# Performance work log

Hardware: AMD Instinct MI355X
Metric: run time of the kernel (lower is better)

The kernel has to match this reference:

```python
import jax, jax.numpy as jnp
import numpy as np

ENC = 1024
DEC = 1024


def setup_inputs() -> dict:
    key = jax.random.key(0)
    k = jax.random.split(key, 8)
    s1 = 1.0 / np.sqrt(ENC)
    s2 = 1.0 / np.sqrt(DEC)
    return {
        "encoder_outputs": jax.random.normal(k[0], (32, 2048, ENC), jnp.float32),
        "decoder_output": jax.random.normal(k[1], (32, 1, DEC), jnp.float32),
        "w1": jax.random.uniform(k[2], (ENC, ENC), jnp.float32, -s1, s1),
        "b1": jax.random.uniform(k[3], (ENC,), jnp.float32, -s1, s1),
        "w2": jax.random.uniform(k[4], (DEC, ENC), jnp.float32, -s2, s2),
        "b2": jax.random.uniform(k[5], (ENC,), jnp.float32, -s2, s2),
        "v": jax.random.uniform(k[6], (ENC, 1), jnp.float32, -s1, s1),
        "bv": jax.random.uniform(k[7], (1,), jnp.float32, -s1, s1),
    }


def reference(encoder_outputs, decoder_output, w1, b1, w2, b2, v, bv):
    # [B,1,E] query projection, broadcast-added to [B,S,E] key projection
    w2_dec = jnp.einsum("bqd,de->bqe", decoder_output, w2) + b2
    w1_enc = jnp.einsum("bsd,de->bse", encoder_outputs, w1) + b1
    scores = jnp.einsum("bse,eo->bso", jnp.tanh(w1_enc + w2_dec), v) + bv  # [B,S,1]
    attn = jax.nn.softmax(scores[..., 0], axis=1)  # softmax over sequence dim
    context = jnp.einsum("bs,bse->be", attn, encoder_outputs)  # [B,E]
    return context
```

## Files before the change

kernel.cpp:

```cpp
#include <hip/hip_runtime.h>
#include <hip/hip_bf16.h>


typedef __attribute__((ext_vector_type(8))) short short8;
typedef __attribute__((ext_vector_type(4))) float f32x4;

#define M_TOTAL 65536
#define KDIM    1024

static __device__ inline unsigned int pk2h(float a, float b) {
    unsigned int ua = __builtin_bit_cast(unsigned int, a) + 0x8000u;
    unsigned int ub = __builtin_bit_cast(unsigned int, b) + 0x8000u;
    return __builtin_amdgcn_perm(ub, ua, 0x07060302u);
}

static __device__ inline uint4 pkvec(float4 f0, float4 f1) {
    uint4 pv;
    pv.x = pk2h(f0.x, f0.y);
    pv.y = pk2h(f0.z, f0.w);
    pv.z = pk2h(f1.x, f1.y);
    pv.w = pk2h(f1.z, f1.w);
    return pv;
}

__global__ __launch_bounds__(64) void pack_w1(const float* __restrict__ w1,
                                              unsigned short* __restrict__ w1p) {
    const int nt = blockIdx.x;
    const int kt = blockIdx.y;
    const int l  = threadIdx.x;
    const int n  = nt * 16 + (l & 15);
    const int kb = kt * 32 + (l >> 4) * 8;
    const float* s = w1 + (size_t)kb * 1024 + n;
    uint4 wv;
    wv.x = pk2h(s[0],    s[1024]);
    wv.y = pk2h(s[2048], s[3072]);
    wv.z = pk2h(s[4096], s[5120]);
    wv.w = pk2h(s[6144], s[7168]);
    *reinterpret_cast<uint4*>(w1p + (((size_t)(kt * 64 + nt)) << 9) + (l << 3)) = wv;
}

__global__ __launch_bounds__(256) void qq_kern(const float* __restrict__ dec,
                                               const float* __restrict__ w2,
                                               const float* __restrict__ b1,
                                               const float* __restrict__ b2,
                                               float* __restrict__ qq) {
    const int b = blockIdx.y;
    const int e = blockIdx.x * 256 + threadIdx.x;
    const int d0 = blockIdx.z * 256;
    const float* db = dec + b * 1024;
    float acc = (blockIdx.z == 0) ? (b1[e] + b2[e]) : 0.f;
#pragma unroll 8
    for (int d = d0; d < d0 + 256; d++)
        acc = fmaf(db[d], w2[d * 1024 + e], acc);
    atomicAdd(&qq[b * 1024 + e], acc);
}

__global__ __launch_bounds__(512, 2) void score_gemm(const float* __restrict__ enc,
                                                     const unsigned short* __restrict__ w1p,
                                                     const float* __restrict__ qq,
                                                     const float* __restrict__ vvec,
                                                     float* __restrict__ scores) {
    __shared__ __align__(16) unsigned short As[2][64 * 256];

    const int m0 = blockIdx.x << 6;
    const int b = m0 >> 11;
    const int tid = threadIdx.x;
    const int wid = tid >> 6;
    const int lane = tid & 63;
    const int quad = lane >> 4, lc = lane & 15;

    const int sr  = tid >> 3;
    const int sc8 = tid & 7;
    const float* srcrow = enc + (size_t)(m0 + sr) * 1024 + (sc8 << 3);
    const int dstoff = (sr << 8) + ((sc8 ^ (sr & 7)) << 3);

    f32x4 acc[4][8];
#pragma unroll
    for (int mi = 0; mi < 4; mi++)
#pragma unroll
        for (int ni = 0; ni < 8; ni++)
            acc[mi][ni] = (f32x4){0.f, 0.f, 0.f, 0.f};

    const unsigned short* bb = w1p + ((size_t)wid << 12) + (lane << 3);

    short8 bA[8], bB[8];
#pragma unroll
    for (int ni = 0; ni < 8; ni++)
        bA[ni] = *reinterpret_cast<const short8*>(bb + ni * 512);

    {
        float4 f0 = *reinterpret_cast<const float4*>(srcrow);
        float4 f1 = *reinterpret_cast<const float4*>(srcrow + 4);
        float4 f2 = *reinterpret_cast<const float4*>(srcrow + 64);
        float4 f3 = *reinterpret_cast<const float4*>(srcrow + 68);
        *reinterpret_cast<uint4*>(&As[0][dstoff])      = pkvec(f0, f1);
        *reinterpret_cast<uint4*>(&As[0][dstoff + 64]) = pkvec(f2, f3);
        f0 = *reinterpret_cast<const float4*>(srcrow + 128);
        f1 = *reinterpret_cast<const float4*>(srcrow + 132);
        f2 = *reinterpret_cast<const float4*>(srcrow + 192);
        f3 = *reinterpret_cast<const float4*>(srcrow + 196);
        *reinterpret_cast<uint4*>(&As[0][dstoff + 128]) = pkvec(f0, f1);
        *reinterpret_cast<uint4*>(&As[0][dstoff + 192]) = pkvec(f2, f3);
    }
    __syncthreads();

    for (int c = 0; c < 4; ++c) {
        const unsigned short* Ar = As[c & 1];
        unsigned short* Aw = const_cast<unsigned short*>(As[(c & 1) ^ 1]);
        const int more = (c < 3);
        const float* snext = srcrow + ((c + 1) << 8);

        float4 fv0, fv1, fv2, fv3;
        if (more) {
            fv0 = *reinterpret_cast<const float4*>(snext);
            fv1 = *reinterpret_cast<const float4*>(snext + 4);
            fv2 = *reinterpret_cast<const float4*>(snext + 64);
            fv3 = *reinterpret_cast<const float4*>(snext + 68);
        }

#pragma unroll
        for (int half = 0; half < 2; ++half) {
#pragma unroll
            for (int it = 0; it < 2; ++it) {
                const int lk = half * 4 + it * 2;
                const int kt = c * 8 + lk;
#pragma unroll
                for (int ni = 0; ni < 8; ni++)
                    bB[ni] = *reinterpret_cast<const short8*>(bb + (kt + 1) * 32768 + ni * 512);

                short8 af[4];
                {
                    const int cc = lk * 4 + quad;
                    const int off = ((cc & ~7) | ((cc ^ lc) & 7)) << 3;
#pragma unroll
                    for (int mi = 0; mi < 4; mi++)
                        af[mi] = *reinterpret_cast<const short8*>(&Ar[((mi * 16 + lc) << 8) + off]);
                }
                __builtin_amdgcn_s_setprio(1);
#pragma unroll
                for (int mi = 0; mi < 4; mi++)
#pragma unroll
                    for (int ni = 0; ni < 8; ni++)
                        acc[mi][ni] = __builtin_amdgcn_mfma_f32_16x16x32_bf16(af[mi], bA[ni], acc[mi][ni], 0, 0, 0);
                __builtin_amdgcn_s_setprio(0);

                if (kt < 30) {
#pragma unroll
                    for (int ni = 0; ni < 8; ni++)
                        bA[ni] = *reinterpret_cast<const short8*>(bb + (kt + 2) * 32768 + ni * 512);
                }
                {
                    const int cc = (lk + 1) * 4 + quad;
                    const int off = ((cc & ~7) | ((cc ^ lc) & 7)) << 3;
#pragma unroll
                    for (int mi = 0; mi < 4; mi++)
                        af[mi] = *reinterpret_cast<const short8*>(&Ar[((mi * 16 + lc) << 8) + off]);
                }
                __builtin_amdgcn_s_setprio(1);
#pragma unroll
                for (int mi = 0; mi < 4; mi++)
#pragma unroll
                    for (int ni = 0; ni < 8; ni++)
                        acc[mi][ni] = __builtin_amdgcn_mfma_f32_16x16x32_bf16(af[mi], bB[ni], acc[mi][ni], 0, 0, 0);
                __builtin_amdgcn_s_setprio(0);
            }

            if (more) {
                if (half == 0) {
                    *reinterpret_cast<uint4*>(&Aw[dstoff])      = pkvec(fv0, fv1);
                    *reinterpret_cast<uint4*>(&Aw[dstoff + 64]) = pkvec(fv2, fv3);
                    fv0 = *reinterpret_cast<const float4*>(snext + 128);
                    fv1 = *reinterpret_cast<const float4*>(snext + 132);
                    fv2 = *reinterpret_cast<const float4*>(snext + 192);
                    fv3 = *reinterpret_cast<const float4*>(snext + 196);
                } else {
                    *reinterpret_cast<uint4*>(&Aw[dstoff + 128]) = pkvec(fv0, fv1);
                    *reinterpret_cast<uint4*>(&Aw[dstoff + 192]) = pkvec(fv2, fv3);
                }
            }
        }
        __syncthreads();
    }

    const float* qb = qq + (b << 10) + (wid << 7) + lc;
    const float* vb = vvec + (wid << 7) + lc;
    float qn[8], vn[8];
#pragma unroll
    for (int ni = 0; ni < 8; ni++) {
        qn[ni] = qb[ni << 4];
        vn[ni] = vb[ni << 4];
    }
    float red[16];
#pragma unroll
    for (int mi = 0; mi < 4; mi++) {
#pragma unroll
        for (int r = 0; r < 4; r++) {
            float ssum = 0.f;
#pragma unroll
            for (int ni = 0; ni < 8; ni++) {
                float x = acc[mi][ni][r] + qn[ni];
                float e = __expf(2.0f * x);
                float th = 1.0f - 2.0f / (e + 1.0f);
                ssum = fmaf(th, vn[ni], ssum);
            }
            float t = ssum;
            t += __shfl_xor(t, 1);
            t += __shfl_xor(t, 2);
            t += __shfl_xor(t, 4);
            t += __shfl_xor(t, 8);
            red[mi * 4 + r] = t;
        }
    }
    float myv = red[0];
#pragma unroll
    for (int i = 1; i < 16; i++)
        if (lc == i) myv = red[i];
    atomicAdd(scores + m0 + (lc >> 2) * 16 + quad * 4 + (lc & 3), myv);
}

__global__ __launch_bounds__(256) void softmax_kern(const float* __restrict__ scores,
                                                    float* __restrict__ attn) {
    const int b = blockIdx.x;
    const int tid = threadIdx.x;
    const int wid = tid >> 6, lane = tid & 63;
    const float* s = scores + b * 2048;
    float x[8];
    float m = -1e30f;
#pragma unroll
    for (int i = 0; i < 8; i++) {
        x[i] = s[tid + i * 256];
        m = fmaxf(m, x[i]);
    }
    for (int off = 1; off < 64; off <<= 1) m = fmaxf(m, __shfl_xor(m, off));
    __shared__ float redm[4];
    if (lane == 0) redm[wid] = m;
    __syncthreads();
    m = fmaxf(fmaxf(redm[0], redm[1]), fmaxf(redm[2], redm[3]));
    float sum = 0.f;
#pragma unroll
    for (int i = 0; i < 8; i++) {
        x[i] = __expf(x[i] - m);
        sum += x[i];
    }
    for (int off = 1; off < 64; off <<= 1) sum += __shfl_xor(sum, off);
    __shared__ float reds[4];
    if (lane == 0) reds[wid] = sum;
    __syncthreads();
    sum = reds[0] + reds[1] + reds[2] + reds[3];
    const float inv = 1.0f / sum;
#pragma unroll
    for (int i = 0; i < 8; i++) attn[b * 2048 + tid + i * 256] = x[i] * inv;
}

__global__ __launch_bounds__(256) void ctx_part(const float* __restrict__ attn,
                                                const float* __restrict__ enc,
                                                float* __restrict__ part) {
    const int b = blockIdx.y;
    const int sc = blockIdx.x;
    const int tid = threadIdx.x;
    const float* ab = attn + b * 2048 + sc * 64;
    const float* eb = enc + ((size_t)b * 2048 + sc * 64) * 1024 + tid * 4;
    float4 acc = {0.f, 0.f, 0.f, 0.f};
#pragma unroll 16
    for (int s = 0; s < 64; s++) {
        float w = ab[s];
        float4 ev = *reinterpret_cast<const float4*>(eb + (size_t)s * 1024);
        acc.x = fmaf(w, ev.x, acc.x);
        acc.y = fmaf(w, ev.y, acc.y);
        acc.z = fmaf(w, ev.z, acc.z);
        acc.w = fmaf(w, ev.w, acc.w);
    }
    *reinterpret_cast<float4*>(part + (((size_t)(sc * 32 + b)) << 10) + tid * 4) = acc;
}

__global__ __launch_bounds__(256) void ctx_reduce(const float* __restrict__ part,
                                                  float* __restrict__ out) {
    const int b = blockIdx.x;
    const int tid = threadIdx.x;
    const float* p = part + ((size_t)b << 10) + tid * 4;
    float4 acc = {0.f, 0.f, 0.f, 0.f};
#pragma unroll
    for (int sc = 0; sc < 32; sc++) {
        float4 v = *reinterpret_cast<const float4*>(p + ((size_t)sc << 15));
        acc.x += v.x; acc.y += v.y; acc.z += v.z; acc.w += v.w;
    }
    *reinterpret_cast<float4*>(out + b * 1024 + tid * 4) = acc;
}

extern "C" void kernel_launch(void* const* d_in, const int* in_sizes, int n_in,
                              void* d_out, int out_size, void* d_ws, size_t ws_size,
                              hipStream_t stream) {
    const float* enc = (const float*)d_in[0];
    const float* dec = (const float*)d_in[1];
    const float* w1  = (const float*)d_in[2];
    const float* b1  = (const float*)d_in[3];
    const float* w2  = (const float*)d_in[4];
    const float* b2  = (const float*)d_in[5];
    const float* v   = (const float*)d_in[6];
    float* out = (float*)d_out;

    char* ws = (char*)d_ws;
    unsigned short* w1p = (unsigned short*)ws;
    float* qq     = (float*)(ws + (2u << 20));
    float* scores = (float*)(ws + (2u << 20) + (128u << 10));
    float* attn   = scores + M_TOTAL;
    float* part   = attn + M_TOTAL;

    hipMemsetAsync(qq, 0, (128u << 10) + M_TOTAL * sizeof(float), stream);

    pack_w1<<<dim3(64, 32), 64, 0, stream>>>(w1, w1p);
    qq_kern<<<dim3(4, 32, 4), 256, 0, stream>>>(dec, w2, b1, b2, qq);
    score_gemm<<<1024, 512, 0, stream>>>(enc, w1p, qq, v, scores);
    softmax_kern<<<32, 256, 0, stream>>>(scores, attn);
    ctx_part<<<dim3(32, 32), 256, 0, stream>>>(attn, enc, part);
    ctx_reduce<<<32, 256, 0, stream>>>(part, out);
}
```

Before: 530.3 us.

## Fuse prep kernels, fold softmax into context, drop atomics and memset

Merges the w1 bf16 packing and the query projection into one prep kernel. The query projection now writes per-split partials instead of atomically accumulating, so the memset can go. The score GEMM sums those partials itself, reduces scores across warps through shared memory instead of using atomics, and drops the s_setprio hints. Softmax moves into ctx_part, where each block recomputes the row max and sum, so one launch and the attn buffer go away. The cost is redundant softmax reductions in every ctx block and four extra qq loads per GEMM block.

```diff
diff --git a/kernel.cpp b/kernel.cpp
--- a/kernel.cpp
+++ b/kernel.cpp
@@ -23,41 +23,47 @@
     return pv;
 }
 
-__global__ __launch_bounds__(64) void pack_w1(const float* __restrict__ w1,
-                                              unsigned short* __restrict__ w1p) {
-    const int nt = blockIdx.x;
-    const int kt = blockIdx.y;
-    const int l  = threadIdx.x;
-    const int n  = nt * 16 + (l & 15);
-    const int kb = kt * 32 + (l >> 4) * 8;
-    const float* s = w1 + (size_t)kb * 1024 + n;
-    uint4 wv;
-    wv.x = pk2h(s[0],    s[1024]);
-    wv.y = pk2h(s[2048], s[3072]);
-    wv.z = pk2h(s[4096], s[5120]);
-    wv.w = pk2h(s[6144], s[7168]);
-    *reinterpret_cast<uint4*>(w1p + (((size_t)(kt * 64 + nt)) << 9) + (l << 3)) = wv;
-}
-
-__global__ __launch_bounds__(256) void qq_kern(const float* __restrict__ dec,
-                                               const float* __restrict__ w2,
-                                               const float* __restrict__ b1,
-                                               const float* __restrict__ b2,
-                                               float* __restrict__ qq) {
-    const int b = blockIdx.y;
-    const int e = blockIdx.x * 256 + threadIdx.x;
-    const int d0 = blockIdx.z * 256;
-    const float* db = dec + b * 1024;
-    float acc = (blockIdx.z == 0) ? (b1[e] + b2[e]) : 0.f;
+__global__ __launch_bounds__(256) void prep_kern(const float* __restrict__ w1,
+                                                 const float* __restrict__ dec,
+                                                 const float* __restrict__ w2,
+                                                 const float* __restrict__ b1,
+                                                 const float* __restrict__ b2,
+                                                 unsigned short* __restrict__ w1p,
+                                                 float* __restrict__ qqp) {
+    const int tid = threadIdx.x;
+    if (blockIdx.x < 512) {
+        const int idx = blockIdx.x * 4 + (tid >> 6);
+        const int l   = tid & 63;
+        const int nt  = idx & 63;
+        const int kt  = idx >> 6;
+        const int n   = nt * 16 + (l & 15);
+        const int kb  = kt * 32 + (l >> 4) * 8;
+        const float* s = w1 + (size_t)kb * 1024 + n;
+        uint4 wv;
+        wv.x = pk2h(s[0],    s[1024]);
+        wv.y = pk2h(s[2048], s[3072]);
+        wv.z = pk2h(s[4096], s[5120]);
+        wv.w = pk2h(s[6144], s[7168]);
+        *reinterpret_cast<uint4*>(w1p + (((size_t)(kt * 64 + nt)) << 9) + (l << 3)) = wv;
+    } else {
+        const int q    = blockIdx.x - 512;
+        const int eblk = q & 3;
+        const int b    = (q >> 2) & 31;
+        const int z    = q >> 7;
+        const int e    = eblk * 256 + tid;
+        const int d0   = z * 256;
+        const float* db = dec + b * 1024;
+        float acc = (z == 0) ? (b1[e] + b2[e]) : 0.f;
 #pragma unroll 8
-    for (int d = d0; d < d0 + 256; d++)
-        acc = fmaf(db[d], w2[d * 1024 + e], acc);
-    atomicAdd(&qq[b * 1024 + e], acc);
+        for (int d = d0; d < d0 + 256; d++)
+            acc = fmaf(db[d], w2[d * 1024 + e], acc);
+        qqp[((z * 32 + b) << 10) + e] = acc;
+    }
 }
 
 __global__ __launch_bounds__(512, 2) void score_gemm(const float* __restrict__ enc,
                                                      const unsigned short* __restrict__ w1p,
-                                                     const float* __restrict__ qq,
+                                                     const float* __restrict__ qqp,
                                                      const float* __restrict__ vvec,
                                                      float* __restrict__ scores) {
     __shared__ __align__(16) unsigned short As[2][64 * 256];
@@ -136,13 +142,11 @@
                     for (int mi = 0; mi < 4; mi++)
                         af[mi] = *reinterpret_cast<const short8*>(&Ar[((mi * 16 + lc) << 8) + off]);
                 }
-                __builtin_amdgcn_s_setprio(1);
 #pragma unroll
                 for (int mi = 0; mi < 4; mi++)
 #pragma unroll
                     for (int ni = 0; ni < 8; ni++)
                         acc[mi][ni] = __builtin_amdgcn_mfma_f32_16x16x32_bf16(af[mi], bA[ni], acc[mi][ni], 0, 0, 0);
-                __builtin_amdgcn_s_setprio(0);
 
                 if (kt < 30) {
 #pragma unroll
@@ -156,13 +160,11 @@
                     for (int mi = 0; mi < 4; mi++)
                         af[mi] = *reinterpret_cast<const short8*>(&Ar[((mi * 16 + lc) << 8) + off]);
                 }
-                __builtin_amdgcn_s_setprio(1);
 #pragma unroll
                 for (int mi = 0; mi < 4; mi++)
 #pragma unroll
                     for (int ni = 0; ni < 8; ni++)
                         acc[mi][ni] = __builtin_amdgcn_mfma_f32_16x16x32_bf16(af[mi], bB[ni], acc[mi][ni], 0, 0, 0);
-                __builtin_amdgcn_s_setprio(0);
             }
 
             if (more) {
@@ -182,12 +184,17 @@
         __syncthreads();
     }
 
-    const float* qb = qq + (b << 10) + (wid << 7) + lc;
-    const float* vb = vvec + (wid << 7) + lc;
+    const int nb0 = (wid << 7) + lc;
+    const float* vb = vvec + nb0;
     float qn[8], vn[8];
 #pragma unroll
     for (int ni = 0; ni < 8; ni++) {
-        qn[ni] = qb[ni << 4];
+        const int nb = nb0 + (ni << 4);
+        float qv = 0.f;
+#pragma unroll
+        for (int z = 0; z < 4; z++)
+            qv += qqp[((z * 32 + b) << 10) + nb];
+        qn[ni] = qv;
         vn[ni] = vb[ni << 4];
     }
     float red[16];
@@ -215,56 +222,59 @@
 #pragma unroll
     for (int i = 1; i < 16; i++)
         if (lc == i) myv = red[i];
-    atomicAdd(scores + m0 + (lc >> 2) * 16 + quad * 4 + (lc & 3), myv);
-}
-
-__global__ __launch_bounds__(256) void softmax_kern(const float* __restrict__ scores,
-                                                    float* __restrict__ attn) {
-    const int b = blockIdx.x;
-    const int tid = threadIdx.x;
-    const int wid = tid >> 6, lane = tid & 63;
-    const float* s = scores + b * 2048;
-    float x[8];
-    float m = -1e30f;
-#pragma unroll
-    for (int i = 0; i < 8; i++) {
-        x[i] = s[tid + i * 256];
-        m = fmaxf(m, x[i]);
-    }
-    for (int off = 1; off < 64; off <<= 1) m = fmaxf(m, __shfl_xor(m, off));
-    __shared__ float redm[4];
-    if (lane == 0) redm[wid] = m;
-    __syncthreads();
-    m = fmaxf(fmaxf(redm[0], redm[1]), fmaxf(redm[2], redm[3]));
-    float sum = 0.f;
-#pragma unroll
-    for (int i = 0; i < 8; i++) {
-        x[i] = __expf(x[i] - m);
-        sum += x[i];
-    }
-    for (int off = 1; off < 64; off <<= 1) sum += __shfl_xor(sum, off);
-    __shared__ float reds[4];
-    if (lane == 0) reds[wid] = sum;
-    __syncthreads();
-    sum = reds[0] + reds[1] + reds[2] + reds[3];
-    const float inv = 1.0f / sum;
-#pragma unroll
-    for (int i = 0; i < 8; i++) attn[b * 2048 + tid + i * 256] = x[i] * inv;
-}
-
-__global__ __launch_bounds__(256) void ctx_part(const float* __restrict__ attn,
+    float* sred = (float*)As;
+    sred[(wid << 6) + (lc >> 2) * 16 + quad * 4 + (lc & 3)] = myv;
+    __syncthreads();
+    if (tid < 64) {
+        float t = 0.f;
+#pragma unroll
+        for (int w = 0; w < 8; w++)
+            t += sred[(w << 6) + tid];
+        scores[m0 + tid] = t;
+    }
+}
+
+__global__ __launch_bounds__(256) void ctx_part(const float* __restrict__ scores,
                                                 const float* __restrict__ enc,
                                                 float* __restrict__ part) {
     const int b = blockIdx.y;
     const int sc = blockIdx.x;
     const int tid = threadIdx.x;
-    const float* ab = attn + b * 2048 + sc * 64;
+    const int wid = tid >> 6, lane = tid & 63;
+    const float* s = scores + b * 2048;
+
+    float x[8];
+    float m = -1e30f;
+#pragma unroll
+    for (int i = 0; i < 8; i++) {
+        x[i] = s[tid + i * 256];
+        m = fmaxf(m, x[i]);
+    }
+    for (int off = 1; off < 64; off <<= 1) m = fmaxf(m, __shfl_xor(m, off));
+    __shared__ float redm[4];
+    if (lane == 0) redm[wid] = m;
+    __syncthreads();
+    m = fmaxf(fmaxf(redm[0], redm[1]), fmaxf(redm[2], redm[3]));
+    float sum = 0.f;
+#pragma unroll
+    for (int i = 0; i < 8; i++) sum += __expf(x[i] - m);
+    for (int off = 1; off < 64; off <<= 1) sum += __shfl_xor(sum, off);
+    __shared__ float reds[4];
+    if (lane == 0) reds[wid] = sum;
+    __syncthreads();
+    sum = reds[0] + reds[1] + reds[2] + reds[3];
+    const float inv = 1.0f / sum;
+
+    __shared__ float attn_s[64];
+    if (tid < 64) attn_s[tid] = __expf(s[sc * 64 + tid] - m) * inv;
+    __syncthreads();
+
     const float* eb = enc + ((size_t)b * 2048 + sc * 64) * 1024 + tid * 4;
     float4 acc = {0.f, 0.f, 0.f, 0.f};
 #pragma unroll 16
-    for (int s = 0; s < 64; s++) {
-        float w = ab[s];
-        float4 ev = *reinterpret_cast<const float4*>(eb + (size_t)s * 1024);
+    for (int si = 0; si < 64; si++) {
+        float w = attn_s[si];
+        float4 ev = *reinterpret_cast<const float4*>(eb + (size_t)si * 1024);
         acc.x = fmaf(w, ev.x, acc.x);
         acc.y = fmaf(w, ev.y, acc.y);
         acc.z = fmaf(w, ev.z, acc.z);
@@ -301,17 +311,12 @@
 
     char* ws = (char*)d_ws;
     unsigned short* w1p = (unsigned short*)ws;
-    float* qq     = (float*)(ws + (2u << 20));
-    float* scores = (float*)(ws + (2u << 20) + (128u << 10));
-    float* attn   = scores + M_TOTAL;
-    float* part   = attn + M_TOTAL;
-
-    hipMemsetAsync(qq, 0, (128u << 10) + M_TOTAL * sizeof(float), stream);
-
-    pack_w1<<<dim3(64, 32), 64, 0, stream>>>(w1, w1p);
-    qq_kern<<<dim3(4, 32, 4), 256, 0, stream>>>(dec, w2, b1, b2, qq);
-    score_gemm<<<1024, 512, 0, stream>>>(enc, w1p, qq, v, scores);
-    softmax_kern<<<32, 256, 0, stream>>>(scores, attn);
-    ctx_part<<<dim3(32, 32), 256, 0, stream>>>(attn, enc, part);
+    float* qqp    = (float*)(ws + (2u << 20));
+    float* scores = (float*)(ws + (2u << 20) + (512u << 10));
+    float* part   = scores + M_TOTAL;
+
+    prep_kern<<<1024, 256, 0, stream>>>(w1, dec, w2, b1, b2, w1p, qqp);
+    score_gemm<<<1024, 512, 0, stream>>>(enc, w1p, qqp, v, scores);
+    ctx_part<<<dim3(32, 32), 256, 0, stream>>>(scores, enc, part);
     ctx_reduce<<<32, 256, 0, stream>>>(part, out);
 }
```

New measurement: 576.0 us. +8.6%, slower.
